# Optimization experiments

Measured on AMD Instinct MI355X. Metric: run time of the kernel, lower is better.

Reference implementation:

```python
import jax, jax.numpy as jnp
import numpy as np

B, S, D_IN, D_OUT, H = 4, 2048, 1024, 1024, 16
HD = D_OUT // H  # 64


def setup_inputs() -> dict:
    key = jax.random.key(0)
    ks = jax.random.split(key, 6)
    scale_in = 1.0 / np.sqrt(D_IN)
    scale_out = 1.0 / np.sqrt(D_OUT)
    return {
        "x": jax.random.normal(ks[0], (B, S, D_IN), dtype=jnp.float32),
        "Wq": jax.random.normal(ks[1], (D_IN, D_OUT), dtype=jnp.float32) * scale_in,
        "Wk": jax.random.normal(ks[2], (D_IN, D_OUT), dtype=jnp.float32) * scale_in,
        "Wv": jax.random.normal(ks[3], (D_IN, D_OUT), dtype=jnp.float32) * scale_in,
        "Wo": jax.random.normal(ks[4], (D_OUT, D_OUT), dtype=jnp.float32) * scale_out,
        "bo": jax.random.normal(ks[5], (D_OUT,), dtype=jnp.float32) * 0.01,
    }


def reference(x, Wq, Wk, Wv, Wo, bo):
    b, s, _ = x.shape
    # project and split heads: (b, s, d_out) -> (b, h, s, hd)
    def split(t):
        return t.reshape(b, s, H, HD).transpose(0, 2, 1, 3)
    q = split(x @ Wq)
    k = split(x @ Wk)
    v = split(x @ Wv)
    # scaled causal attention scores (b, h, s, s)
    scores = jnp.einsum('bhqd,bhkd->bhqk', q, k) / jnp.sqrt(jnp.float32(HD))
    causal = jnp.tril(jnp.ones((s, s), dtype=bool))
    scores = jnp.where(causal, scores, -jnp.inf)
    weights = jax.nn.softmax(scores, axis=-1)
    # dropout p=0.0 -> identity (eval mode)
    ctx = jnp.einsum('bhqk,bhkd->bhqd', weights, v)
    ctx = ctx.transpose(0, 2, 1, 3).reshape(b, s, D_OUT)
    return ctx @ Wo + bo
```

## Files before the change

### kernel.cpp

```cpp
#include <hip/hip_runtime.h>
#include <stdint.h>

#define DEVINL __device__ __forceinline__

typedef __attribute__((ext_vector_type(8))) __bf16 bf16x8;
typedef __attribute__((ext_vector_type(4))) float f32x4;
typedef __attribute__((ext_vector_type(8))) unsigned short u16x8;
typedef __attribute__((ext_vector_type(2))) unsigned int u32x2;

constexpr int Bc = 4, Sc = 2048, DINc = 1024, Hc = 16;
constexpr float QSCALE = 0.18033688011112042f;

DEVINL unsigned short f2bf(float x) {
  unsigned u = __builtin_bit_cast(unsigned, x);
  u += 0x7fffu + ((u >> 16) & 1u);
  return (unsigned short)(u >> 16);
}

DEVINL unsigned pack_bf16_trunc(float p0, float p1) {
  return __builtin_amdgcn_perm(__builtin_bit_cast(unsigned, p1),
                               __builtin_bit_cast(unsigned, p0), 0x07060302u);
}

DEVINL void gload_lds16(const void* g, void* l) {
  __builtin_amdgcn_global_load_lds(
      (const __attribute__((address_space(1))) void*)g,
      (__attribute__((address_space(3))) void*)l, 16, 0, 0);
}

template <int ROWS>
DEVINL void stage_tile(const unsigned short* g, int ld, void* lds, int tid) {
#pragma unroll
  for (int p = 0; p < ROWS / 32; ++p) {
    int L = (p * 256 + tid) * 16;
    int row = L >> 7;
    int cb = L & 127;
    int scb = cb ^ ((row & 7) << 4);
    gload_lds16((const char*)(g + (size_t)row * ld) + scb, (char*)lds + L);
  }
}

DEVINL bf16x8 read_frag(const void* lds, int row, int kelem) {
  int addr = row * 128 + (((kelem * 2) ^ ((row & 7) << 4)));
  return *(const bf16x8*)((const char*)lds + addr);
}

__global__ __launch_bounds__(256) void cvt_bf16(const float* __restrict__ in,
                                                unsigned short* __restrict__ out,
                                                int n) {
  int i = (blockIdx.x * 256 + threadIdx.x) * 8;
  if (i + 8 > n) return;
  f32x4 a = *(const f32x4*)(in + i);
  f32x4 b = *(const f32x4*)(in + i + 4);
  u16x8 r;
  r[0] = f2bf(a[0]); r[1] = f2bf(a[1]); r[2] = f2bf(a[2]); r[3] = f2bf(a[3]);
  r[4] = f2bf(b[0]); r[5] = f2bf(b[1]); r[6] = f2bf(b[2]); r[7] = f2bf(b[3]);
  *(u16x8*)(out + i) = r;
}

__global__ __launch_bounds__(256) void transpose_convert4(
    const float* __restrict__ Wq, const float* __restrict__ Wk,
    const float* __restrict__ Wv, const float* __restrict__ Wo,
    unsigned short* __restrict__ wqkvt, unsigned short* __restrict__ wot) {
  __shared__ float t[64][65];
  const float* src;
  unsigned short* dst;
  int z = blockIdx.z;
  if (z == 0)      { src = Wq; dst = wqkvt; }
  else if (z == 1) { src = Wk; dst = wqkvt + (size_t)1024 * 1024; }
  else if (z == 2) { src = Wv; dst = wqkvt + (size_t)2048 * 1024; }
  else             { src = Wo; dst = wot; }
  int n0 = blockIdx.x * 64, k0 = blockIdx.y * 64;
  int tx = threadIdx.x & 63, ty = threadIdx.x >> 6;
#pragma unroll
  for (int r = 0; r < 64; r += 4)
    t[r + ty][tx] = src[(size_t)(k0 + r + ty) * 1024 + n0 + tx];
  __syncthreads();
#pragma unroll
  for (int r = 0; r < 64; r += 4)
    dst[(size_t)(n0 + r + ty) * 1024 + k0 + tx] = f2bf(t[tx][r + ty]);
}

__global__ __launch_bounds__(256, 2) void gemm_qkv(
    const unsigned short* __restrict__ A, const unsigned short* __restrict__ Bt,
    unsigned short* __restrict__ qws, unsigned short* __restrict__ kws,
    unsigned short* __restrict__ vtws) {
  __shared__ __align__(16) char lsmem[4 * 128 * 64 * 2];
  unsigned short* lA0 = (unsigned short*)lsmem;
  unsigned short* lB0 = (unsigned short*)(lsmem + 32768);
  int tid = threadIdx.x, lane = tid & 63, wave = tid >> 6;
  int wr = wave >> 1, wc = wave & 1;
  int bm = blockIdx.x, bn = blockIdx.y;
  const unsigned short* Ab = A + (size_t)bm * 128 * 1024;
  const unsigned short* Bb = Bt + (size_t)bn * 128 * 1024;
  int r15 = lane & 15, g4 = lane >> 4, khi = g4 * 8;

  f32x4 acc[4][4];
#pragma unroll
  for (int i = 0; i < 4; ++i)
#pragma unroll
    for (int j = 0; j < 4; ++j) acc[i][j] = (f32x4){0.f, 0.f, 0.f, 0.f};

  int cur = 0;
  stage_tile<128>(Ab, 1024, lA0, tid);
  stage_tile<128>(Bb, 1024, lB0, tid);
#pragma unroll 1
  for (int t = 0; t < 16; ++t) {
    __syncthreads();
    if (t + 1 < 16) {
      stage_tile<128>(Ab + (t + 1) * 64, 1024, lA0 + (cur ^ 1) * 128 * 64, tid);
      stage_tile<128>(Bb + (t + 1) * 64, 1024, lB0 + (cur ^ 1) * 128 * 64, tid);
    }
#pragma unroll
    for (int ks = 0; ks < 2; ++ks) {
      bf16x8 af[4], bfr[4];
#pragma unroll
      for (int i = 0; i < 4; ++i)
        af[i] = read_frag(lA0 + cur * 128 * 64, wr * 64 + i * 16 + r15, ks * 32 + khi);
#pragma unroll
      for (int j = 0; j < 4; ++j)
        bfr[j] = read_frag(lB0 + cur * 128 * 64, wc * 64 + j * 16 + r15, ks * 32 + khi);
      __builtin_amdgcn_s_setprio(1);
#pragma unroll
      for (int i = 0; i < 4; ++i)
#pragma unroll
        for (int j = 0; j < 4; ++j)
          acc[i][j] = __builtin_amdgcn_mfma_f32_16x16x32_bf16(af[i], bfr[j], acc[i][j], 0, 0, 0);
      __builtin_amdgcn_s_setprio(0);
    }
    cur ^= 1;
  }

  int sel = bn >> 3;
  float* sc = (float*)lsmem;
  constexpr int PADW = 132;
  int bq = (bm * 128) >> 11;
#pragma unroll 1
  for (int pass = 0; pass < 2; ++pass) {
    __syncthreads();
    if (wr == pass) {
#pragma unroll
      for (int i = 0; i < 4; ++i)
#pragma unroll
        for (int j = 0; j < 4; ++j)
#pragma unroll
          for (int r = 0; r < 4; ++r) {
            float v = acc[i][j][r];
            if (sel == 0) v *= QSCALE;
            sc[(i * 16 + g4 * 4 + r) * PADW + wc * 64 + j * 16 + r15] = v;
          }
    }
    __syncthreads();
    if (sel < 2) {
      int row = tid >> 2, c0 = (tid & 3) * 32;
      int m = bm * 128 + pass * 64 + row;
      int s = m & 2047;
      int colg = (bn & 7) * 128 + c0;
      int h = colg >> 6, d0 = colg & 63;
      unsigned short* dst =
          (sel == 0 ? qws : kws) + ((size_t)(bq * 16 + h) * 2048 + s) * 64 + d0;
#pragma unroll
      for (int q = 0; q < 4; ++q) {
        f32x4 a = *(const f32x4*)&sc[row * PADW + c0 + q * 8];
        f32x4 b2 = *(const f32x4*)&sc[row * PADW + c0 + q * 8 + 4];
        u16x8 o;
        o[0] = f2bf(a[0]);  o[1] = f2bf(a[1]);  o[2] = f2bf(a[2]);  o[3] = f2bf(a[3]);
        o[4] = f2bf(b2[0]); o[5] = f2bf(b2[1]); o[6] = f2bf(b2[2]); o[7] = f2bf(b2[3]);
        *(u16x8*)(dst + q * 8) = o;
      }
    } else {
      int col = tid >> 1, s0loc = (tid & 1) * 32;
      int colg = (bn & 7) * 128 + col;
      int h = colg >> 6, d = colg & 63;
      int sbase = (bm * 128 + pass * 64 + s0loc) & 2047;
      unsigned short* dst =
          vtws + ((size_t)(bq * 16 + h) * 64 + d) * 2048 + sbase;
#pragma unroll
      for (int q = 0; q < 4; ++q) {
        u16x8 o;
#pragma unroll
        for (int e = 0; e < 8; ++e)
          o[e] = f2bf(sc[(s0loc + q * 8 + e) * PADW + col]);
        *(u16x8*)(dst + q * 8) = o;
      }
    }
  }
}

__global__ __launch_bounds__(256, 3) void attn(
    const unsigned short* __restrict__ qws, const unsigned short* __restrict__ kws,
    const unsigned short* __restrict__ vtws, unsigned short* __restrict__ ctx) {
  __shared__ __align__(16) unsigned short lK[2][64 * 64];
  __shared__ __align__(16) unsigned short lV[2][64 * 64];
  __shared__ __align__(16) unsigned short lP[4][32 * 64];
  int tid = threadIdx.x, lane = tid & 63, wave = tid >> 6;
  int bh = blockIdx.x * 8 + (blockIdx.y & 7);
  int t = 15 - (int)(blockIdx.y >> 3);
  int r15 = lane & 15, g4 = lane >> 4;
  const unsigned short* Kb = kws + (size_t)bh * 2048 * 64;
  const unsigned short* Vb = vtws + (size_t)bh * 64 * 2048;
  int b = bh >> 4, h = bh & 15;
  char* Pw = (char*)&lP[wave][0];

  int q0 = t * 128;
  int myrow0 = q0 + wave * 32;
  const unsigned short* Qb = qws + ((size_t)bh * 2048 + myrow0) * 64;

  bf16x8 qf[2][2];
#pragma unroll
  for (int mf = 0; mf < 2; ++mf)
#pragma unroll
    for (int ks = 0; ks < 2; ++ks)
      qf[mf][ks] = *(const bf16x8*)(Qb + (size_t)(mf * 16 + r15) * 64 + ks * 32 + g4 * 8);

  float m_run[2] = {-1e30f, -1e30f}, l_run[2] = {0.f, 0.f};
  f32x4 o_acc[2][4];
#pragma unroll
  for (int mf = 0; mf < 2; ++mf)
#pragma unroll
    for (int df = 0; df < 4; ++df) o_acc[mf][df] = (f32x4){0.f, 0.f, 0.f, 0.f};

  int nkt = 2 * t + 2;
  int cur = 0;
  stage_tile<64>(Kb, 64, lK[0], tid);
  stage_tile<64>(Vb, 2048, lV[0], tid);

#pragma unroll 1
  for (int kt = 0; kt < nkt; ++kt) {
    __syncthreads();
    if (kt + 1 < nkt) {
      stage_tile<64>(Kb + (size_t)(kt + 1) * 64 * 64, 64, lK[cur ^ 1], tid);
      stage_tile<64>(Vb + (size_t)(kt + 1) * 64, 2048, lV[cur ^ 1], tid);
    }

    f32x4 sacc[2][4];
#pragma unroll
    for (int mf = 0; mf < 2; ++mf)
#pragma unroll
      for (int nf = 0; nf < 4; ++nf) sacc[mf][nf] = (f32x4){0.f, 0.f, 0.f, 0.f};
#pragma unroll
    for (int ks = 0; ks < 2; ++ks) {
      bf16x8 kf[4];
#pragma unroll
      for (int nf = 0; nf < 4; ++nf)
        kf[nf] = read_frag(lK[cur], nf * 16 + r15, ks * 32 + g4 * 8);
      __builtin_amdgcn_s_setprio(1);
#pragma unroll
      for (int mf = 0; mf < 2; ++mf)
#pragma unroll
        for (int nf = 0; nf < 4; ++nf)
          sacc[mf][nf] = __builtin_amdgcn_mfma_f32_16x16x32_bf16(kf[nf], qf[mf][ks], sacc[mf][nf], 0, 0, 0);
      __builtin_amdgcn_s_setprio(0);
    }

    if (kt * 64 + 63 > myrow0) {
#pragma unroll
      for (int mf = 0; mf < 2; ++mf) {
        int q = myrow0 + mf * 16 + r15;
#pragma unroll
        for (int nf = 0; nf < 4; ++nf) {
          int kbase = kt * 64 + nf * 16 + g4 * 4;
#pragma unroll
          for (int r = 0; r < 4; ++r)
            if (kbase + r > q) sacc[mf][nf][r] = -3e38f;
        }
      }
    }

    float tm[2];
#pragma unroll
    for (int mf = 0; mf < 2; ++mf) {
      float a0 = fmaxf(fmaxf(sacc[mf][0][0], sacc[mf][0][1]), fmaxf(sacc[mf][0][2], sacc[mf][0][3]));
      float a1 = fmaxf(fmaxf(sacc[mf][1][0], sacc[mf][1][1]), fmaxf(sacc[mf][1][2], sacc[mf][1][3]));
      float a2 = fmaxf(fmaxf(sacc[mf][2][0], sacc[mf][2][1]), fmaxf(sacc[mf][2][2], sacc[mf][2][3]));
      float a3 = fmaxf(fmaxf(sacc[mf][3][0], sacc[mf][3][1]), fmaxf(sacc[mf][3][2], sacc[mf][3][3]));
      float m = fmaxf(fmaxf(a0, a1), fmaxf(a2, a3));
      m = fmaxf(m, __shfl_xor(m, 16));
      m = fmaxf(m, __shfl_xor(m, 32));
      tm[mf] = m;
    }

    bool ok = (tm[0] <= m_run[0] + 11.5f) & (tm[1] <= m_run[1] + 11.5f);
    if (!__all(ok)) {
#pragma unroll
      for (int mf = 0; mf < 2; ++mf) {
        float mn = fmaxf(m_run[mf], tm[mf]);
        float a = __builtin_amdgcn_exp2f(m_run[mf] - mn);
        m_run[mf] = mn;
        l_run[mf] *= a;
        float av[4];
#pragma unroll
        for (int r = 0; r < 4; ++r)
          av[r] = __shfl(a, (g4 * 4 + r) | (lane & 48));
#pragma unroll
        for (int df = 0; df < 4; ++df)
#pragma unroll
          for (int r = 0; r < 4; ++r) o_acc[mf][df][r] *= av[r];
      }
    }

    float rs[2] = {0.f, 0.f};
#pragma unroll
    for (int mf = 0; mf < 2; ++mf) {
      int prow = mf * 16 + r15;
      char* Prow = Pw + prow * 128;
      int sw = (prow & 7) << 4;
#pragma unroll
      for (int nf = 0; nf < 4; ++nf) {
        float p0 = __builtin_amdgcn_exp2f(sacc[mf][nf][0] - m_run[mf]);
        float p1 = __builtin_amdgcn_exp2f(sacc[mf][nf][1] - m_run[mf]);
        float p2 = __builtin_amdgcn_exp2f(sacc[mf][nf][2] - m_run[mf]);
        float p3 = __builtin_amdgcn_exp2f(sacc[mf][nf][3] - m_run[mf]);
        rs[mf] += (p0 + p1) + (p2 + p3);
        *(u32x2*)(Prow + (((nf * 16 + g4 * 4) * 2) ^ sw)) =
            (u32x2){pack_bf16_trunc(p0, p1), pack_bf16_trunc(p2, p3)};
      }
      float s = rs[mf];
      s += __shfl_xor(s, 16);
      s += __shfl_xor(s, 32);
      l_run[mf] += s;
    }

#pragma unroll
    for (int ks = 0; ks < 2; ++ks) {
      bf16x8 vf[4];
#pragma unroll
      for (int df = 0; df < 4; ++df)
        vf[df] = read_frag(lV[cur], df * 16 + r15, ks * 32 + g4 * 8);
      bf16x8 pf[2];
#pragma unroll
      for (int mf = 0; mf < 2; ++mf)
        pf[mf] = read_frag(Pw, mf * 16 + r15, ks * 32 + g4 * 8);
      __builtin_amdgcn_s_setprio(1);
#pragma unroll
      for (int mf = 0; mf < 2; ++mf)
#pragma unroll
        for (int df = 0; df < 4; ++df)
          o_acc[mf][df] = __builtin_amdgcn_mfma_f32_16x16x32_bf16(pf[mf], vf[df], o_acc[mf][df], 0, 0, 0);
      __builtin_amdgcn_s_setprio(0);
    }
    cur ^= 1;
  }

#pragma unroll
  for (int mf = 0; mf < 2; ++mf) {
    float rl = 1.f / l_run[mf];
    float rv[4];
#pragma unroll
    for (int r = 0; r < 4; ++r)
      rv[r] = __shfl(rl, (g4 * 4 + r) | (lane & 48));
#pragma unroll
    for (int r = 0; r < 4; ++r) {
      int row = myrow0 + mf * 16 + g4 * 4 + r;
#pragma unroll
      for (int df = 0; df < 4; ++df)
        ctx[((size_t)(b * 2048 + row)) * 1024 + h * 64 + df * 16 + r15] =
            f2bf(o_acc[mf][df][r] * rv[r]);
    }
  }
}

__global__ __launch_bounds__(256, 2) void gemm_out(
    const unsigned short* __restrict__ A, const unsigned short* __restrict__ Bt,
    const float* __restrict__ bo, float* __restrict__ out) {
  __shared__ __align__(16) unsigned short lA[2][128 * 64];
  __shared__ __align__(16) unsigned short lB[2][128 * 64];
  int tid = threadIdx.x, lane = tid & 63, wave = tid >> 6;
  int wr = wave >> 1, wc = wave & 1;
  int bm = blockIdx.x, bn = blockIdx.y;
  const unsigned short* Ab = A + (size_t)bm * 128 * 1024;
  const unsigned short* Bb = Bt + (size_t)bn * 128 * 1024;
  int r15 = lane & 15, khi = (lane >> 4) * 8;

  f32x4 acc[4][4];
#pragma unroll
  for (int i = 0; i < 4; ++i)
#pragma unroll
    for (int j = 0; j < 4; ++j) acc[i][j] = (f32x4){0.f, 0.f, 0.f, 0.f};

  int cur = 0;
  stage_tile<128>(Ab, 1024, lA[0], tid);
  stage_tile<128>(Bb, 1024, lB[0], tid);
#pragma unroll 1
  for (int t = 0; t < 16; ++t) {
    __syncthreads();
    if (t + 1 < 16) {
      stage_tile<128>(Ab + (t + 1) * 64, 1024, lA[cur ^ 1], tid);
      stage_tile<128>(Bb + (t + 1) * 64, 1024, lB[cur ^ 1], tid);
    }
#pragma unroll
    for (int ks = 0; ks < 2; ++ks) {
      bf16x8 af[4], bfr[4];
#pragma unroll
      for (int i = 0; i < 4; ++i)
        af[i] = read_frag(lA[cur], wr * 64 + i * 16 + r15, ks * 32 + khi);
#pragma unroll
      for (int j = 0; j < 4; ++j)
        bfr[j] = read_frag(lB[cur], wc * 64 + j * 16 + r15, ks * 32 + khi);
      __builtin_amdgcn_s_setprio(1);
#pragma unroll
      for (int i = 0; i < 4; ++i)
#pragma unroll
        for (int j = 0; j < 4; ++j)
          acc[i][j] = __builtin_amdgcn_mfma_f32_16x16x32_bf16(af[i], bfr[j], acc[i][j], 0, 0, 0);
      __builtin_amdgcn_s_setprio(0);
    }
    cur ^= 1;
  }

  int nbase = bn * 128 + wc * 64;
  int mbase = bm * 128 + wr * 64;
#pragma unroll
  for (int j = 0; j < 4; ++j) {
    int n = nbase + j * 16 + r15;
    float bias = bo[n];
#pragma unroll
    for (int i = 0; i < 4; ++i)
#pragma unroll
      for (int r = 0; r < 4; ++r) {
        int m = mbase + i * 16 + (lane >> 4) * 4 + r;
        out[(size_t)m * 1024 + n] = acc[i][j][r] + bias;
      }
  }
}

extern "C" void kernel_launch(void* const* d_in, const int* in_sizes, int n_in,
                              void* d_out, int out_size, void* d_ws, size_t ws_size,
                              hipStream_t stream) {
  const float* x = (const float*)d_in[0];
  const float* Wq = (const float*)d_in[1];
  const float* Wk = (const float*)d_in[2];
  const float* Wv = (const float*)d_in[3];
  const float* Wo = (const float*)d_in[4];
  const float* bo = (const float*)d_in[5];
  float* out = (float*)d_out;

  char* ws = (char*)d_ws;
  unsigned short* xb    = (unsigned short*)(ws);
  unsigned short* wqkvt = (unsigned short*)(ws + (16u << 20));
  unsigned short* wot   = (unsigned short*)(ws + (22u << 20));
  unsigned short* qws   = (unsigned short*)(ws + (24u << 20));
  unsigned short* kws   = (unsigned short*)(ws + (40u << 20));
  unsigned short* vtws  = (unsigned short*)(ws + (56u << 20));
  unsigned short* ctxws = (unsigned short*)(ws + (72u << 20));

  cvt_bf16<<<dim3(4096), dim3(256), 0, stream>>>(x, xb, Bc * Sc * DINc);
  transpose_convert4<<<dim3(16, 16, 4), dim3(256), 0, stream>>>(Wq, Wk, Wv, Wo, wqkvt, wot);

  gemm_qkv<<<dim3(64, 24), dim3(256), 0, stream>>>(xb, wqkvt, qws, kws, vtws);
  attn<<<dim3(8, 128), dim3(256), 0, stream>>>(qws, kws, vtws, ctxws);
  gemm_out<<<dim3(64, 8), dim3(256), 0, stream>>>(ctxws, wot, bo, out);
}
```

Measured before the change: 168.4 us.

## Use 512-thread attention blocks covering 256 query rows to share K/V tiles

The attention kernel now runs 8 waves per block over 256 query rows instead of 4 waves over 128, so each staged K/V tile in LDS serves twice as many query rows and global K/V traffic per query drops. Waves whose rows end before the current key tile skip compute but still join the barriers. Query tiles are ordered in a new interleaved way for load balance. The cost is more idle waves on causal diagonal tiles, fewer blocks in flight, and a larger per-block LDS footprint.

After: 190.5 us. +13.1%, slower.

```diff
diff --git a/kernel.cpp b/kernel.cpp
--- a/kernel.cpp
+++ b/kernel.cpp
@@ -28,11 +28,11 @@
       (__attribute__((address_space(3))) void*)l, 16, 0, 0);
 }
 
-template <int ROWS>
+template <int ROWS, int THREADS>
 DEVINL void stage_tile(const unsigned short* g, int ld, void* lds, int tid) {
 #pragma unroll
-  for (int p = 0; p < ROWS / 32; ++p) {
-    int L = (p * 256 + tid) * 16;
+  for (int p = 0; p < (ROWS * 128) / (THREADS * 16); ++p) {
+    int L = (p * THREADS + tid) * 16;
     int row = L >> 7;
     int cb = L & 127;
     int scb = cb ^ ((row & 7) << 4);
@@ -102,14 +102,14 @@
     for (int j = 0; j < 4; ++j) acc[i][j] = (f32x4){0.f, 0.f, 0.f, 0.f};
 
   int cur = 0;
-  stage_tile<128>(Ab, 1024, lA0, tid);
-  stage_tile<128>(Bb, 1024, lB0, tid);
+  stage_tile<128, 256>(Ab, 1024, lA0, tid);
+  stage_tile<128, 256>(Bb, 1024, lB0, tid);
 #pragma unroll 1
   for (int t = 0; t < 16; ++t) {
     __syncthreads();
     if (t + 1 < 16) {
-      stage_tile<128>(Ab + (t + 1) * 64, 1024, lA0 + (cur ^ 1) * 128 * 64, tid);
-      stage_tile<128>(Bb + (t + 1) * 64, 1024, lB0 + (cur ^ 1) * 128 * 64, tid);
+      stage_tile<128, 256>(Ab + (t + 1) * 64, 1024, lA0 + (cur ^ 1) * 128 * 64, tid);
+      stage_tile<128, 256>(Bb + (t + 1) * 64, 1024, lB0 + (cur ^ 1) * 128 * 64, tid);
     }
 #pragma unroll
     for (int ks = 0; ks < 2; ++ks) {
@@ -187,23 +187,25 @@
   }
 }
 
-__global__ __launch_bounds__(256, 3) void attn(
+__global__ __launch_bounds__(512, 2) void attn(
     const unsigned short* __restrict__ qws, const unsigned short* __restrict__ kws,
     const unsigned short* __restrict__ vtws, unsigned short* __restrict__ ctx) {
   __shared__ __align__(16) unsigned short lK[2][64 * 64];
   __shared__ __align__(16) unsigned short lV[2][64 * 64];
-  __shared__ __align__(16) unsigned short lP[4][32 * 64];
+  __shared__ __align__(16) unsigned short lP[8][32 * 64];
   int tid = threadIdx.x, lane = tid & 63, wave = tid >> 6;
+  int j = (int)(blockIdx.y >> 3);
+  int t2 = (j < 4) ? (7 - j) : (j - 4);
   int bh = blockIdx.x * 8 + (blockIdx.y & 7);
-  int t = 15 - (int)(blockIdx.y >> 3);
   int r15 = lane & 15, g4 = lane >> 4;
   const unsigned short* Kb = kws + (size_t)bh * 2048 * 64;
   const unsigned short* Vb = vtws + (size_t)bh * 64 * 2048;
   int b = bh >> 4, h = bh & 15;
   char* Pw = (char*)&lP[wave][0];
 
-  int q0 = t * 128;
-  int myrow0 = q0 + wave * 32;
+  int myrow0 = t2 * 256 + wave * 32;
+  int nkt_blk = 4 * t2 + 4;
+  int nkt_w = (myrow0 >> 6) + 1;
   const unsigned short* Qb = qws + ((size_t)bh * 2048 + myrow0) * 64;
 
   bf16x8 qf[2][2];
@@ -220,124 +222,125 @@
 #pragma unroll
     for (int df = 0; df < 4; ++df) o_acc[mf][df] = (f32x4){0.f, 0.f, 0.f, 0.f};
 
-  int nkt = 2 * t + 2;
   int cur = 0;
-  stage_tile<64>(Kb, 64, lK[0], tid);
-  stage_tile<64>(Vb, 2048, lV[0], tid);
+  stage_tile<64, 512>(Kb, 64, lK[0], tid);
+  stage_tile<64, 512>(Vb, 2048, lV[0], tid);
 
 #pragma unroll 1
-  for (int kt = 0; kt < nkt; ++kt) {
+  for (int kt = 0; kt < nkt_blk; ++kt) {
     __syncthreads();
-    if (kt + 1 < nkt) {
-      stage_tile<64>(Kb + (size_t)(kt + 1) * 64 * 64, 64, lK[cur ^ 1], tid);
-      stage_tile<64>(Vb + (size_t)(kt + 1) * 64, 2048, lV[cur ^ 1], tid);
-    }
-
-    f32x4 sacc[2][4];
-#pragma unroll
-    for (int mf = 0; mf < 2; ++mf)
-#pragma unroll
-      for (int nf = 0; nf < 4; ++nf) sacc[mf][nf] = (f32x4){0.f, 0.f, 0.f, 0.f};
-#pragma unroll
-    for (int ks = 0; ks < 2; ++ks) {
-      bf16x8 kf[4];
-#pragma unroll
-      for (int nf = 0; nf < 4; ++nf)
-        kf[nf] = read_frag(lK[cur], nf * 16 + r15, ks * 32 + g4 * 8);
-      __builtin_amdgcn_s_setprio(1);
+    if (kt + 1 < nkt_blk) {
+      stage_tile<64, 512>(Kb + (size_t)(kt + 1) * 64 * 64, 64, lK[cur ^ 1], tid);
+      stage_tile<64, 512>(Vb + (size_t)(kt + 1) * 64, 2048, lV[cur ^ 1], tid);
+    }
+
+    if (kt < nkt_w) {
+      f32x4 sacc[2][4];
 #pragma unroll
       for (int mf = 0; mf < 2; ++mf)
 #pragma unroll
+        for (int nf = 0; nf < 4; ++nf) sacc[mf][nf] = (f32x4){0.f, 0.f, 0.f, 0.f};
+#pragma unroll
+      for (int ks = 0; ks < 2; ++ks) {
+        bf16x8 kf[4];
+#pragma unroll
         for (int nf = 0; nf < 4; ++nf)
-          sacc[mf][nf] = __builtin_amdgcn_mfma_f32_16x16x32_bf16(kf[nf], qf[mf][ks], sacc[mf][nf], 0, 0, 0);
-      __builtin_amdgcn_s_setprio(0);
-    }
-
-    if (kt * 64 + 63 > myrow0) {
+          kf[nf] = read_frag(lK[cur], nf * 16 + r15, ks * 32 + g4 * 8);
+        __builtin_amdgcn_s_setprio(1);
+#pragma unroll
+        for (int mf = 0; mf < 2; ++mf)
+#pragma unroll
+          for (int nf = 0; nf < 4; ++nf)
+            sacc[mf][nf] = __builtin_amdgcn_mfma_f32_16x16x32_bf16(kf[nf], qf[mf][ks], sacc[mf][nf], 0, 0, 0);
+        __builtin_amdgcn_s_setprio(0);
+      }
+
+      if (kt * 64 + 63 > myrow0) {
+#pragma unroll
+        for (int mf = 0; mf < 2; ++mf) {
+          int q = myrow0 + mf * 16 + r15;
+#pragma unroll
+          for (int nf = 0; nf < 4; ++nf) {
+            int kbase = kt * 64 + nf * 16 + g4 * 4;
+#pragma unroll
+            for (int r = 0; r < 4; ++r)
+              if (kbase + r > q) sacc[mf][nf][r] = -3e38f;
+          }
+        }
+      }
+
+      float tm[2];
 #pragma unroll
       for (int mf = 0; mf < 2; ++mf) {
-        int q = myrow0 + mf * 16 + r15;
+        float a0 = fmaxf(fmaxf(sacc[mf][0][0], sacc[mf][0][1]), fmaxf(sacc[mf][0][2], sacc[mf][0][3]));
+        float a1 = fmaxf(fmaxf(sacc[mf][1][0], sacc[mf][1][1]), fmaxf(sacc[mf][1][2], sacc[mf][1][3]));
+        float a2 = fmaxf(fmaxf(sacc[mf][2][0], sacc[mf][2][1]), fmaxf(sacc[mf][2][2], sacc[mf][2][3]));
+        float a3 = fmaxf(fmaxf(sacc[mf][3][0], sacc[mf][3][1]), fmaxf(sacc[mf][3][2], sacc[mf][3][3]));
+        float m = fmaxf(fmaxf(a0, a1), fmaxf(a2, a3));
+        m = fmaxf(m, __shfl_xor(m, 16));
+        m = fmaxf(m, __shfl_xor(m, 32));
+        tm[mf] = m;
+      }
+
+      bool ok = (tm[0] <= m_run[0] + 11.5f) & (tm[1] <= m_run[1] + 11.5f);
+      if (!__all(ok)) {
+#pragma unroll
+        for (int mf = 0; mf < 2; ++mf) {
+          float mn = fmaxf(m_run[mf], tm[mf]);
+          float a = __builtin_amdgcn_exp2f(m_run[mf] - mn);
+          m_run[mf] = mn;
+          l_run[mf] *= a;
+          float av[4];
+#pragma unroll
+          for (int r = 0; r < 4; ++r)
+            av[r] = __shfl(a, (g4 * 4 + r) | (lane & 48));
+#pragma unroll
+          for (int df = 0; df < 4; ++df)
+#pragma unroll
+            for (int r = 0; r < 4; ++r) o_acc[mf][df][r] *= av[r];
+        }
+      }
+
+      float rs[2] = {0.f, 0.f};
+#pragma unroll
+      for (int mf = 0; mf < 2; ++mf) {
+        int prow = mf * 16 + r15;
+        char* Prow = Pw + prow * 128;
+        int sw = (prow & 7) << 4;
 #pragma unroll
         for (int nf = 0; nf < 4; ++nf) {
-          int kbase = kt * 64 + nf * 16 + g4 * 4;
-#pragma unroll
-          for (int r = 0; r < 4; ++r)
-            if (kbase + r > q) sacc[mf][nf][r] = -3e38f;
+          float p0 = __builtin_amdgcn_exp2f(sacc[mf][nf][0] - m_run[mf]);
+          float p1 = __builtin_amdgcn_exp2f(sacc[mf][nf][1] - m_run[mf]);
+          float p2 = __builtin_amdgcn_exp2f(sacc[mf][nf][2] - m_run[mf]);
+          float p3 = __builtin_amdgcn_exp2f(sacc[mf][nf][3] - m_run[mf]);
+          rs[mf] += (p0 + p1) + (p2 + p3);
+          *(u32x2*)(Prow + (((nf * 16 + g4 * 4) * 2) ^ sw)) =
+              (u32x2){pack_bf16_trunc(p0, p1), pack_bf16_trunc(p2, p3)};
         }
-      }
-    }
-
-    float tm[2];
-#pragma unroll
-    for (int mf = 0; mf < 2; ++mf) {
-      float a0 = fmaxf(fmaxf(sacc[mf][0][0], sacc[mf][0][1]), fmaxf(sacc[mf][0][2], sacc[mf][0][3]));
-      float a1 = fmaxf(fmaxf(sacc[mf][1][0], sacc[mf][1][1]), fmaxf(sacc[mf][1][2], sacc[mf][1][3]));
-      float a2 = fmaxf(fmaxf(sacc[mf][2][0], sacc[mf][2][1]), fmaxf(sacc[mf][2][2], sacc[mf][2][3]));
-      float a3 = fmaxf(fmaxf(sacc[mf][3][0], sacc[mf][3][1]), fmaxf(sacc[mf][3][2], sacc[mf][3][3]));
-      float m = fmaxf(fmaxf(a0, a1), fmaxf(a2, a3));
-      m = fmaxf(m, __shfl_xor(m, 16));
-      m = fmaxf(m, __shfl_xor(m, 32));
-      tm[mf] = m;
-    }
-
-    bool ok = (tm[0] <= m_run[0] + 11.5f) & (tm[1] <= m_run[1] + 11.5f);
-    if (!__all(ok)) {
-#pragma unroll
-      for (int mf = 0; mf < 2; ++mf) {
-        float mn = fmaxf(m_run[mf], tm[mf]);
-        float a = __builtin_amdgcn_exp2f(m_run[mf] - mn);
-        m_run[mf] = mn;
-        l_run[mf] *= a;
-        float av[4];
-#pragma unroll
-        for (int r = 0; r < 4; ++r)
-          av[r] = __shfl(a, (g4 * 4 + r) | (lane & 48));
+        float s = rs[mf];
+        s += __shfl_xor(s, 16);
+        s += __shfl_xor(s, 32);
+        l_run[mf] += s;
+      }
+
+#pragma unroll
+      for (int ks = 0; ks < 2; ++ks) {
+        bf16x8 vf[4];
 #pragma unroll
         for (int df = 0; df < 4; ++df)
-#pragma unroll
-          for (int r = 0; r < 4; ++r) o_acc[mf][df][r] *= av[r];
-      }
-    }
-
-    float rs[2] = {0.f, 0.f};
-#pragma unroll
-    for (int mf = 0; mf < 2; ++mf) {
-      int prow = mf * 16 + r15;
-      char* Prow = Pw + prow * 128;
-      int sw = (prow & 7) << 4;
-#pragma unroll
-      for (int nf = 0; nf < 4; ++nf) {
-        float p0 = __builtin_amdgcn_exp2f(sacc[mf][nf][0] - m_run[mf]);
-        float p1 = __builtin_amdgcn_exp2f(sacc[mf][nf][1] - m_run[mf]);
-        float p2 = __builtin_amdgcn_exp2f(sacc[mf][nf][2] - m_run[mf]);
-        float p3 = __builtin_amdgcn_exp2f(sacc[mf][nf][3] - m_run[mf]);
-        rs[mf] += (p0 + p1) + (p2 + p3);
-        *(u32x2*)(Prow + (((nf * 16 + g4 * 4) * 2) ^ sw)) =
-            (u32x2){pack_bf16_trunc(p0, p1), pack_bf16_trunc(p2, p3)};
-      }
-      float s = rs[mf];
-      s += __shfl_xor(s, 16);
-      s += __shfl_xor(s, 32);
-      l_run[mf] += s;
-    }
-
-#pragma unroll
-    for (int ks = 0; ks < 2; ++ks) {
-      bf16x8 vf[4];
-#pragma unroll
-      for (int df = 0; df < 4; ++df)
-        vf[df] = read_frag(lV[cur], df * 16 + r15, ks * 32 + g4 * 8);
-      bf16x8 pf[2];
-#pragma unroll
-      for (int mf = 0; mf < 2; ++mf)
-        pf[mf] = read_frag(Pw, mf * 16 + r15, ks * 32 + g4 * 8);
-      __builtin_amdgcn_s_setprio(1);
-#pragma unroll
-      for (int mf = 0; mf < 2; ++mf)
-#pragma unroll
-        for (int df = 0; df < 4; ++df)
-          o_acc[mf][df] = __builtin_amdgcn_mfma_f32_16x16x32_bf16(pf[mf], vf[df], o_acc[mf][df], 0, 0, 0);
-      __builtin_amdgcn_s_setprio(0);
+          vf[df] = read_frag(lV[cur], df * 16 + r15, ks * 32 + g4 * 8);
+        bf16x8 pf[2];
+#pragma unroll
+        for (int mf = 0; mf < 2; ++mf)
+          pf[mf] = read_frag(Pw, mf * 16 + r15, ks * 32 + g4 * 8);
+        __builtin_amdgcn_s_setprio(1);
+#pragma unroll
+        for (int mf = 0; mf < 2; ++mf)
+#pragma unroll
+          for (int df = 0; df < 4; ++df)
+            o_acc[mf][df] = __builtin_amdgcn_mfma_f32_16x16x32_bf16(pf[mf], vf[df], o_acc[mf][df], 0, 0, 0);
+        __builtin_amdgcn_s_setprio(0);
+      }
     }
     cur ^= 1;
   }
@@ -379,14 +382,14 @@
     for (int j = 0; j < 4; ++j) acc[i][j] = (f32x4){0.f, 0.f, 0.f, 0.f};
 
   int cur = 0;
-  stage_tile<128>(Ab, 1024, lA[0], tid);
-  stage_tile<128>(Bb, 1024, lB[0], tid);
+  stage_tile<128, 256>(Ab, 1024, lA[0], tid);
+  stage_tile<128, 256>(Bb, 1024, lB[0], tid);
 #pragma unroll 1
   for (int t = 0; t < 16; ++t) {
     __syncthreads();
     if (t + 1 < 16) {
-      stage_tile<128>(Ab + (t + 1) * 64, 1024, lA[cur ^ 1], tid);
-      stage_tile<128>(Bb + (t + 1) * 64, 1024, lB[cur ^ 1], tid);
+      stage_tile<128, 256>(Ab + (t + 1) * 64, 1024, lA[cur ^ 1], tid);
+      stage_tile<128, 256>(Bb + (t + 1) * 64, 1024, lB[cur ^ 1], tid);
     }
 #pragma unroll
     for (int ks = 0; ks < 2; ++ks) {
@@ -448,6 +451,6 @@
   transpose_convert4<<<dim3(16, 16, 4), dim3(256), 0, stream>>>(Wq, Wk, Wv, Wo, wqkvt, wot);
 
   gemm_qkv<<<dim3(64, 24), dim3(256), 0, stream>>>(xb, wqkvt, qws, kws, vtws);
-  attn<<<dim3(8, 128), dim3(256), 0, stream>>>(qws, kws, vtws, ctxws);
+  attn<<<dim3(8, 64), dim3(512), 0, stream>>>(qws, kws, vtws, ctxws);
   gemm_out<<<dim3(64, 8), dim3(256), 0, stream>>>(ctxws, wot, bo, out);
 }
```
